# Kernel optimization log

Hardware: AMD Instinct MI355X
Metric: run time of the kernel (lower is better)

Reference implementation:

```python
import jax, jax.numpy as jnp
import numpy as np

# dims: M=512 new tokens, N=2048 model dim, D=128 head dim, H=16 heads,
# L=4096 cache length, P=2048 cache write offset

def setup_inputs() -> dict:
    key = jax.random.key(0)
    k0, k1, k2, k3 = jax.random.split(key, 4)
    M, N, D, L = 512, 2048, 128, 4096
    X = jax.random.normal(k0, (M, N), jnp.float32)
    # scale weights ~1/sqrt(N) so projections have unit-ish scale
    W_qkv = jax.random.normal(k1, (N, 3 * N), jnp.float32) * (N ** -0.5)
    H = N // D
    cache_K = jax.random.normal(k2, (H, L, D), jnp.float32)
    # realistic cache state: keys stored in cache are RMS-normalized
    cache_K = cache_K * jax.lax.rsqrt(jnp.mean(cache_K * cache_K, axis=-1, keepdims=True))
    cache_V = jax.random.normal(k3, (H, L, D), jnp.float32)
    return {"X": X, "W_qkv": W_qkv, "cache_K": cache_K, "cache_V": cache_V, "P": 2048}


def reference(X, W_qkv, cache_K, cache_V, P):
    M = X.shape[0]
    H, L, D = cache_K.shape
    qkv = X @ W_qkv                              # [M, 3N]
    q, k, v = jnp.split(qkv, 3, axis=-1)         # each [M, N]
    q = q.reshape(M, H, D).transpose(1, 0, 2)    # [H, M, D]
    k = k.reshape(M, H, D).transpose(1, 0, 2)
    v = v.reshape(M, H, D).transpose(1, 0, 2)
    # RMS-style normalization (no learned gain, no eps in original)
    q = q * jax.lax.rsqrt(jnp.mean(q * q, axis=-1, keepdims=True))
    k = k * jax.lax.rsqrt(jnp.mean(k * k, axis=-1, keepdims=True))
    # scatter-update into KV cache at position P
    Kc = jax.lax.dynamic_update_slice(cache_K, k, (0, P, 0))  # [H, L, D]
    Vc = jax.lax.dynamic_update_slice(cache_V, v, (0, P, 0))
    # unmasked, unscaled attention over the full cache (faithful to original:
    # plain exp/sum, no max-subtraction, no 1/sqrt(D))
    scores = jnp.einsum('hmd,hld->hml', q, Kc)   # [H, M, L]
    w = jnp.exp(scores)
    w = w / jnp.sum(w, axis=-1, keepdims=True)
    out = jnp.einsum('hml,hld->hmd', w, Vc)      # [H, M, D]
    return out.transpose(1, 0, 2).reshape(M, H * D)
```

## Files before the change

kernel.cpp:

```cpp
#include <hip/hip_runtime.h>
#include <math.h>

typedef _Float16 half_t;
typedef _Float16 half8 __attribute__((ext_vector_type(8)));
typedef _Float16 half4_t __attribute__((ext_vector_type(4)));
typedef _Float16 half2_t __attribute__((ext_vector_type(2)));
typedef float floatx4 __attribute__((ext_vector_type(4)));

#define M_TOK 512
#define N_DIM 2048
#define D_HEAD 128
#define H_HEADS 16
#define L_CACHE 4096
#define THREE_N 6144
#define NCHUNK 8
#define LCHUNK 512

__global__ __launch_bounds__(256) void prep_kernel(const float* __restrict__ W,
                                                   const float* __restrict__ X,
                                                   half_t* __restrict__ W16T,
                                                   half_t* __restrict__ X16) {
    __shared__ half_t tile[64 * 66];
    int b = blockIdx.x;
    int t = threadIdx.x;

    if (b < 3072) {
        int n0 = (b % 96) * 64, k0 = (b / 96) * 64;
        {
            int k = t >> 2, c0 = (t & 3) * 16;
            const float* src = W + (size_t)(k0 + k) * THREE_N + n0 + c0;
            float4 v[4];
#pragma unroll
            for (int j = 0; j < 4; ++j) v[j] = *(const float4*)(src + j * 4);
#pragma unroll
            for (int j = 0; j < 4; ++j) {
                tile[(c0 + j * 4 + 0) * 66 + k] = (half_t)v[j].x;
                tile[(c0 + j * 4 + 1) * 66 + k] = (half_t)v[j].y;
                tile[(c0 + j * 4 + 2) * 66 + k] = (half_t)v[j].z;
                tile[(c0 + j * 4 + 3) * 66 + k] = (half_t)v[j].w;
            }
        }
        __syncthreads();
        {
            int n = t >> 2, kg = (t & 3) * 16;
            half_t* dst = W16T + (size_t)(n0 + n) * N_DIM + k0 + kg;
            *(half8*)(dst) = *(half8*)&tile[n * 66 + kg];
            *(half8*)(dst + 8) = *(half8*)&tile[n * 66 + kg + 8];
        }
        return;
    }
    b -= 3072;
    {
        size_t i = (size_t)b * 2048 + t * 4;
        float4 v0 = *(const float4*)(X + i);
        float4 v1 = *(const float4*)(X + i + 1024);
        half4_t h0 = {(half_t)v0.x, (half_t)v0.y, (half_t)v0.z, (half_t)v0.w};
        half4_t h1 = {(half_t)v1.x, (half_t)v1.y, (half_t)v1.z, (half_t)v1.w};
        *(half4_t*)(X16 + i) = h0;
        *(half4_t*)(X16 + i + 1024) = h1;
    }
}

__global__ __launch_bounds__(256, 5) void mega_kernel(const half_t* __restrict__ X16,
                                                      const half_t* __restrict__ W16T,
                                                      const float* __restrict__ cK,
                                                      const float* __restrict__ cV,
                                                      const int* __restrict__ Pp,
                                                      half_t* __restrict__ Q16,
                                                      half_t* __restrict__ K16,
                                                      half_t* __restrict__ V16T) {
    __shared__ __align__(16) char smem[20992];
    const int t = threadIdx.x;
    int b = blockIdx.x;

    if (b >= 768) {
        b -= 768;
        const int P = *Pp;
        if (b < 1024) {
            int h = b >> 6, l0 = (b & 63) * 64;
            if (l0 >= P && l0 + 64 <= P + M_TOK) return;
            size_t base = ((size_t)h * L_CACHE + l0) * D_HEAD;
            float4 v[8];
#pragma unroll
            for (int i = 0; i < 8; ++i)
                v[i] = *(const float4*)(cK + base + i * 1024 + t * 4);
#pragma unroll
            for (int i = 0; i < 8; ++i) {
                int row = l0 + ((i * 1024 + t * 4) >> 7);
                half4_t hh = {(half_t)v[i].x, (half_t)v[i].y, (half_t)v[i].z, (half_t)v[i].w};
                if (row < P || row >= P + M_TOK)
                    *(half4_t*)(K16 + base + i * 1024 + t * 4) = hh;
            }
            return;
        }
        b -= 1024;
        {
            int h = b >> 7;
            int rem = b & 127;
            int lt = rem >> 1, dt = rem & 1;
            int l0 = lt * 64, d0 = dt * 64;
            if (l0 >= P && l0 + 64 <= P + M_TOK) return;
            bool overlap = (l0 < P + M_TOK) && (l0 + 64 > P);
            half_t* tile = (half_t*)smem;
            {
                int l = t >> 2, c0 = (t & 3) * 16;
                const float* src = cV + ((size_t)h * L_CACHE + l0 + l) * D_HEAD + d0 + c0;
                float4 v[4];
#pragma unroll
                for (int j = 0; j < 4; ++j) v[j] = *(const float4*)(src + j * 4);
#pragma unroll
                for (int j = 0; j < 4; ++j) {
                    tile[(c0 + j * 4 + 0) * 66 + l] = (half_t)v[j].x;
                    tile[(c0 + j * 4 + 1) * 66 + l] = (half_t)v[j].y;
                    tile[(c0 + j * 4 + 2) * 66 + l] = (half_t)v[j].z;
                    tile[(c0 + j * 4 + 3) * 66 + l] = (half_t)v[j].w;
                }
            }
            __syncthreads();
            {
                int d = t >> 2, lg = (t & 3) * 16;
                half_t* dst = V16T + ((size_t)h * D_HEAD + d0 + d) * L_CACHE + l0 + lg;
                if (!overlap) {
                    *(half8*)(dst) = *(half8*)&tile[d * 66 + lg];
                    *(half8*)(dst + 8) = *(half8*)&tile[d * 66 + lg + 8];
                } else {
#pragma unroll
                    for (int j = 0; j < 16; ++j) {
                        int l = l0 + lg + j;
                        if (l < P || l >= P + M_TOK) dst[j] = tile[d * 66 + lg + j];
                    }
                }
            }
            return;
        }
    }

    half_t* As = (half_t*)smem;
    half_t* Bs = (half_t*)(smem + 4096);
    half_t* Vt = (half_t*)smem;
    float* ssb = (float*)(smem + 20480);
    const int wid = t >> 6, lane = t & 63;
    const int quad = lane >> 4, ln = lane & 15;
    const int bx = b % 48, by = b / 48;
    const int m0 = by * 32, n0 = bx * 128;
    const int wm = (wid >> 1) * 16, wn = (wid & 1) * 64;

    floatx4 acc[4] = {};

    const int ar = t >> 3, ag = (t & 7) * 8;
    const int br = t >> 3, bg = (t & 7) * 8;
    const int rdk = (ln & 7) << 3;

    for (int k0 = 0; k0 < N_DIM; k0 += 64) {
        __syncthreads();
        *(half8*)&As[ar * 64 + (ag ^ ((ar & 7) << 3))] =
            *(const half8*)(X16 + (size_t)(m0 + ar) * N_DIM + k0 + ag);
#pragma unroll
        for (int p = 0; p < 4; ++p) {
            int r = br + p * 32;
            *(half8*)&Bs[r * 64 + (bg ^ ((r & 7) << 3))] =
                *(const half8*)(W16T + (size_t)(n0 + r) * N_DIM + k0 + bg);
        }
        __syncthreads();
#pragma unroll
        for (int kt = 0; kt < 2; ++kt) {
            half8 a, bb[4];
            a = *(half8*)&As[(wm + ln) * 64 + ((kt * 32 + quad * 8) ^ rdk)];
#pragma unroll
            for (int j = 0; j < 4; ++j)
                bb[j] = *(half8*)&Bs[(wn + j * 16 + ln) * 64 + ((kt * 32 + quad * 8) ^ rdk)];
#pragma unroll
            for (int j = 0; j < 4; ++j)
                acc[j] = __builtin_amdgcn_mfma_f32_16x16x32_f16(a, bb[j], acc[j], 0, 0, 0);
        }
    }

    const int seg = bx >> 4, h = bx & 15;
    const int P = *Pp;

    if (seg < 2) {
        float ss[4], scale[4];
#pragma unroll
        for (int r = 0; r < 4; ++r) {
            float s = 0.f;
#pragma unroll
            for (int j = 0; j < 4; ++j) s += acc[j][r] * acc[j][r];
#pragma unroll
            for (int msk = 1; msk < 16; msk <<= 1) s += __shfl_xor(s, msk, 64);
            ss[r] = s;
        }
        if (ln == 0) {
#pragma unroll
            for (int r = 0; r < 4; ++r)
                ssb[wid * 16 + quad * 4 + r] = ss[r];
        }
        __syncthreads();
#pragma unroll
        for (int r = 0; r < 4; ++r)
            scale[r] = rsqrtf((ss[r] + ssb[(wid ^ 1) * 16 + quad * 4 + r]) * (1.0f / 128.0f));
#pragma unroll
        for (int j = 0; j < 4; ++j) {
            int col = wn + j * 16 + ln;
#pragma unroll
            for (int r = 0; r < 4; ++r) {
                int m = m0 + wm + quad * 4 + r;
                half_t val = (half_t)(acc[j][r] * scale[r]);
                if (seg == 0)
                    Q16[((size_t)h * M_TOK + m) * D_HEAD + col] = val;
                else
                    K16[((size_t)h * L_CACHE + P + m) * D_HEAD + col] = val;
            }
        }
    } else {
        __syncthreads();
#pragma unroll
        for (int j = 0; j < 4; ++j) {
            int d = wn + j * 16 + ln;
#pragma unroll
            for (int r = 0; r < 4; ++r)
                Vt[d * 40 + wm + quad * 4 + r] = (half_t)acc[j][r];
        }
        __syncthreads();
#pragma unroll
        for (int p = 0; p < 2; ++p) {
            int s = p * 256 + t;
            int d = s >> 2, sg = s & 3;
            *(half8*)(V16T + ((size_t)h * D_HEAD + d) * L_CACHE + P + m0 + sg * 8) =
                *(half8*)&Vt[d * 40 + sg * 8];
        }
    }
}

__global__ __launch_bounds__(256, 4) void attn_partial_kernel(const half_t* __restrict__ Q16,
                                                              const half_t* __restrict__ K16,
                                                              const half_t* __restrict__ V16T,
                                                              half_t* __restrict__ Opart,
                                                              float* __restrict__ mstat,
                                                              float* __restrict__ lstat) {
    __shared__ half_t Ks[64 * 128];
    __shared__ half_t Vs[128 * 64];
    __shared__ half_t Ps[4 * 16 * 64];
    const int t = threadIdx.x, w = t >> 6, lane = t & 63;
    const int quad = lane >> 4, ln = lane & 15;

    const int bid = blockIdx.x;
    const int xcd = bid & 7, slot = bid >> 3;
    const int pair = (xcd << 4) | (slot >> 3);
    const int h = pair & 15, c = pair >> 4, mi = slot & 7;
    const int mb = mi * 64;

    const half_t* Qh = Q16 + (size_t)h * M_TOK * D_HEAD;
    const half_t* Kh = K16 + (size_t)h * L_CACHE * D_HEAD;
    const half_t* Vh = V16T + (size_t)h * D_HEAD * L_CACHE;

    const int m0 = mb + w * 16;
    half8 qf[4];
#pragma unroll
    for (int dt = 0; dt < 4; ++dt)
        qf[dt] = *(const half8*)(Qh + (size_t)(m0 + ln) * D_HEAD + dt * 32 + quad * 8);

    floatx4 oacc[8] = {};
    float mrow = -INFINITY;
    float lrow = 0.f;

    half_t* Pw = Ps + w * (16 * 64);
    const int psw = (ln & 7) << 3;

    const int l0base = c * LCHUNK;
    const int kr = t >> 4, kc = (t & 15) * 8;
    const int vr = t >> 3, vc = (t & 7) * 8;
    const int ksw = (kr & 7) << 3;
    const int vsw = (vr & 7) << 3;

    half8 kreg[4], vreg[4];
#pragma unroll
    for (int p = 0; p < 4; ++p) {
        kreg[p] = *(const half8*)(Kh + (size_t)(l0base + p * 16 + kr) * D_HEAD + kc);
        vreg[p] = *(const half8*)(Vh + (size_t)(p * 32 + vr) * L_CACHE + l0base + vc);
    }

    for (int it = 0; it < LCHUNK / 64; ++it) {
        __syncthreads();
#pragma unroll
        for (int p = 0; p < 4; ++p)
            *(half8*)&Ks[(p * 16 + kr) * 128 + (kc ^ ksw)] = kreg[p];
#pragma unroll
        for (int p = 0; p < 4; ++p)
            *(half8*)&Vs[(p * 32 + vr) * 64 + (vc ^ vsw)] = vreg[p];
        if (it + 1 < LCHUNK / 64) {
            int l1 = l0base + (it + 1) * 64;
#pragma unroll
            for (int p = 0; p < 4; ++p) {
                kreg[p] = *(const half8*)(Kh + (size_t)(l1 + p * 16 + kr) * D_HEAD + kc);
                vreg[p] = *(const half8*)(Vh + (size_t)(p * 32 + vr) * L_CACHE + l1 + vc);
            }
        }
        __syncthreads();

        floatx4 sacc[4] = {};
#pragma unroll
        for (int dt = 0; dt < 4; ++dt) {
            half8 kf[4];
#pragma unroll
            for (int nt = 0; nt < 4; ++nt)
                kf[nt] = *(half8*)&Ks[(nt * 16 + ln) * 128 + ((dt * 32 + quad * 8) ^ psw)];
#pragma unroll
            for (int nt = 0; nt < 4; ++nt)
                sacc[nt] = __builtin_amdgcn_mfma_f32_16x16x32_f16(kf[nt], qf[dt], sacc[nt], 0, 0, 0);
        }

        {
            float mx = sacc[0][0];
#pragma unroll
            for (int nt = 0; nt < 4; ++nt)
#pragma unroll
                for (int r = 0; r < 4; ++r) mx = fmaxf(mx, sacc[nt][r]);
            mx = fmaxf(mx, __shfl_xor(mx, 16));
            mx = fmaxf(mx, __shfl_xor(mx, 32));
            if (__ballot(mx > mrow)) {
                float mnew = fmaxf(mrow, mx);
                float alpha = __expf(mrow - mnew);
                mrow = mnew;
                lrow *= alpha;
                float ar[4];
#pragma unroll
                for (int r = 0; r < 4; ++r) ar[r] = __shfl(alpha, quad * 4 + r, 16);
#pragma unroll
                for (int nt8 = 0; nt8 < 8; ++nt8)
#pragma unroll
                    for (int r = 0; r < 4; ++r) oacc[nt8][r] *= ar[r];
            }
            float psum = 0.f;
#pragma unroll
            for (int nt = 0; nt < 4; ++nt) {
                half4_t h4;
#pragma unroll
                for (int r = 0; r < 4; ++r) {
                    float p = __expf(sacc[nt][r] - mrow);
                    psum += p;
                    h4[r] = (half_t)p;
                }
                *(half4_t*)&Pw[ln * 64 + ((nt * 16 + quad * 4) ^ psw)] = h4;
            }
            psum += __shfl_xor(psum, 16);
            psum += __shfl_xor(psum, 32);
            lrow += psum;
        }

#pragma unroll
        for (int kt = 0; kt < 2; ++kt) {
            half8 a = *(half8*)&Pw[ln * 64 + ((kt * 32 + quad * 8) ^ psw)];
#pragma unroll
            for (int nt8 = 0; nt8 < 8; ++nt8) {
                half8 b = *(half8*)&Vs[(nt8 * 16 + ln) * 64 + ((kt * 32 + quad * 8) ^ psw)];
                oacc[nt8] = __builtin_amdgcn_mfma_f32_16x16x32_f16(a, b, oacc[nt8], 0, 0, 0);
            }
        }
    }

    half_t* Oc = Opart + ((size_t)(c * H_HEADS + h) * M_TOK) * D_HEAD;
    float* ms = mstat + (size_t)(c * H_HEADS + h) * M_TOK;
    float* ls = lstat + (size_t)(c * H_HEADS + h) * M_TOK;
#pragma unroll
    for (int nt8 = 0; nt8 < 8; ++nt8) {
        int col = nt8 * 16 + ln;
#pragma unroll
        for (int r = 0; r < 4; ++r)
            Oc[(size_t)(m0 + quad * 4 + r) * D_HEAD + col] = (half_t)oacc[nt8][r];
    }
    if (lane < 16) {
        ms[m0 + lane] = mrow;
        ls[m0 + lane] = lrow;
    }
}

__global__ __launch_bounds__(256) void combine_kernel(const half_t* __restrict__ Opart,
                                                      const float* __restrict__ mstat,
                                                      const float* __restrict__ lstat,
                                                      float* __restrict__ out) {
    int gw = blockIdx.x * 4 + (threadIdx.x >> 6);
    int lane = threadIdx.x & 63;
    int h = gw >> 9, m = gw & 511;
    int d = lane * 2;

    float ms[NCHUNK];
    float mg = -INFINITY;
#pragma unroll
    for (int c = 0; c < NCHUNK; ++c) {
        ms[c] = mstat[((c * H_HEADS + h) << 9) + m];
        mg = fmaxf(mg, ms[c]);
    }
    float denom = 0.f, o0 = 0.f, o1 = 0.f;
#pragma unroll
    for (int c = 0; c < NCHUNK; ++c) {
        float e = __expf(ms[c] - mg);
        denom += lstat[((c * H_HEADS + h) << 9) + m] * e;
        const half_t* Oc = Opart + (((size_t)(c * H_HEADS + h) << 9) + m) * D_HEAD + d;
        half2_t v = *(const half2_t*)Oc;
        o0 += (float)v.x * e;
        o1 += (float)v.y * e;
    }
    float inv = 1.0f / denom;
    float* op = out + (size_t)m * N_DIM + h * D_HEAD + d;
    op[0] = o0 * inv;
    op[1] = o1 * inv;
}

extern "C" void kernel_launch(void* const* d_in, const int* in_sizes, int n_in,
                              void* d_out, int out_size, void* d_ws, size_t ws_size,
                              hipStream_t stream) {
    const float* X = (const float*)d_in[0];
    const float* W = (const float*)d_in[1];
    const float* cK = (const float*)d_in[2];
    const float* cV = (const float*)d_in[3];
    const int* Pp = (const int*)d_in[4];
    float* out = (float*)d_out;

    char* ws = (char*)d_ws;
    half_t* Q16 = (half_t*)(ws + 0);
    half_t* K16 = (half_t*)(ws + 2097152);
    half_t* V16T = (half_t*)(ws + 18874368);
    half_t* X16 = (half_t*)(ws + 35651584);
    half_t* W16T = (half_t*)(ws + 37748736);
    half_t* Opart = (half_t*)(ws + 37748736);
    float* mstat = (float*)(ws + 71303168);
    float* lstat = (float*)(ws + 71827456);

    prep_kernel<<<3584, 256, 0, stream>>>(W, X, W16T, X16);
    mega_kernel<<<3840, 256, 0, stream>>>(X16, W16T, cK, cV, Pp, Q16, K16, V16T);
    attn_partial_kernel<<<1024, 256, 0, stream>>>(Q16, K16, V16T, Opart, mstat, lstat);
    combine_kernel<<<2048, 256, 0, stream>>>(Opart, mstat, lstat, out);
}
```

Before: 215.2 us.

## Fuse all stages into one persistent kernel with software grid barriers

Replaces the four separate launches (prep, GEMM+cache convert, attention partial, combine) with a single persistent kernel of 512 blocks that loops over work units and separates stages with atomic-based grid barriers. Within the middle stage, blocks interleave GEMM and cache-conversion work in alternating order so memory-bound and compute-bound work overlap across the device. The aim is to remove launch gaps and tail effects between kernels. In exchange, occupancy is capped at 512 resident blocks with larger shared memory, the barriers spin-wait, and the scheme relies on all blocks being co-resident to avoid deadlock.

```diff
diff --git a/kernel.cpp b/kernel.cpp
--- a/kernel.cpp
+++ b/kernel.cpp
@@ -15,395 +15,436 @@
 #define THREE_N 6144
 #define NCHUNK 8
 #define LCHUNK 512
-
-__global__ __launch_bounds__(256) void prep_kernel(const float* __restrict__ W,
-                                                   const float* __restrict__ X,
-                                                   half_t* __restrict__ W16T,
-                                                   half_t* __restrict__ X16) {
-    __shared__ half_t tile[64 * 66];
-    int b = blockIdx.x;
-    int t = threadIdx.x;
-
-    if (b < 3072) {
-        int n0 = (b % 96) * 64, k0 = (b / 96) * 64;
-        {
-            int k = t >> 2, c0 = (t & 3) * 16;
-            const float* src = W + (size_t)(k0 + k) * THREE_N + n0 + c0;
-            float4 v[4];
-#pragma unroll
-            for (int j = 0; j < 4; ++j) v[j] = *(const float4*)(src + j * 4);
-#pragma unroll
-            for (int j = 0; j < 4; ++j) {
-                tile[(c0 + j * 4 + 0) * 66 + k] = (half_t)v[j].x;
-                tile[(c0 + j * 4 + 1) * 66 + k] = (half_t)v[j].y;
-                tile[(c0 + j * 4 + 2) * 66 + k] = (half_t)v[j].z;
-                tile[(c0 + j * 4 + 3) * 66 + k] = (half_t)v[j].w;
-            }
+#define NBLK 512
+
+__device__ __forceinline__ void grid_bar(int* cnt, int* gen, int k) {
+    __syncthreads();
+    if (threadIdx.x == 0) {
+        int prev = __hip_atomic_fetch_add(cnt, 1, __ATOMIC_ACQ_REL, __HIP_MEMORY_SCOPE_AGENT);
+        if (prev == NBLK - 1) {
+            __hip_atomic_store(cnt, 0, __ATOMIC_RELAXED, __HIP_MEMORY_SCOPE_AGENT);
+            __hip_atomic_store(gen, k + 1, __ATOMIC_RELEASE, __HIP_MEMORY_SCOPE_AGENT);
+        } else {
+            while (__hip_atomic_load(gen, __ATOMIC_RELAXED, __HIP_MEMORY_SCOPE_AGENT) <= k)
+                __builtin_amdgcn_s_sleep(16);
+        }
+        __builtin_amdgcn_fence(__ATOMIC_ACQUIRE, "agent");
+    }
+    __syncthreads();
+}
+
+__global__ __launch_bounds__(256, 2) void fused_kernel(
+    const float* __restrict__ X, const float* __restrict__ W,
+    const float* __restrict__ cK, const float* __restrict__ cV,
+    const int* __restrict__ Pp,
+    half_t* __restrict__ W16T, half_t* __restrict__ X16,
+    half_t* __restrict__ Q16, half_t* __restrict__ K16,
+    half_t* __restrict__ V16T,
+    half_t* __restrict__ Opart, float* __restrict__ mstat,
+    float* __restrict__ lstat, float* __restrict__ out,
+    int* bar_cnt, int* bar_gen) {
+    __shared__ __align__(16) char smem[40960];
+    const int t = threadIdx.x;
+    const int bid = blockIdx.x;
+
+    {
+        half_t* tile = (half_t*)smem;
+        for (int u = bid; u < 3584; u += NBLK) {
+            if (u < 3072) {
+                int n0 = (u % 96) * 64, k0 = (u / 96) * 64;
+                __syncthreads();
+                {
+                    int k = t >> 2, c0 = (t & 3) * 16;
+                    const float* src = W + (size_t)(k0 + k) * THREE_N + n0 + c0;
+                    float4 v[4];
+#pragma unroll
+                    for (int j = 0; j < 4; ++j) v[j] = *(const float4*)(src + j * 4);
+#pragma unroll
+                    for (int j = 0; j < 4; ++j) {
+                        tile[(c0 + j * 4 + 0) * 66 + k] = (half_t)v[j].x;
+                        tile[(c0 + j * 4 + 1) * 66 + k] = (half_t)v[j].y;
+                        tile[(c0 + j * 4 + 2) * 66 + k] = (half_t)v[j].z;
+                        tile[(c0 + j * 4 + 3) * 66 + k] = (half_t)v[j].w;
+                    }
+                }
+                __syncthreads();
+                {
+                    int n = t >> 2, kg = (t & 3) * 16;
+                    half_t* dst = W16T + (size_t)(n0 + n) * N_DIM + k0 + kg;
+                    *(half8*)(dst) = *(half8*)&tile[n * 66 + kg];
+                    *(half8*)(dst + 8) = *(half8*)&tile[n * 66 + kg + 8];
+                }
+            } else {
+                int b = u - 3072;
+                size_t i = (size_t)b * 2048 + t * 4;
+                float4 v0 = *(const float4*)(X + i);
+                float4 v1 = *(const float4*)(X + i + 1024);
+                half4_t h0 = {(half_t)v0.x, (half_t)v0.y, (half_t)v0.z, (half_t)v0.w};
+                half4_t h1 = {(half_t)v1.x, (half_t)v1.y, (half_t)v1.z, (half_t)v1.w};
+                *(half4_t*)(X16 + i) = h0;
+                *(half4_t*)(X16 + i + 1024) = h1;
+            }
+        }
+    }
+    grid_bar(bar_cnt, bar_gen, 0);
+
+    {
+        const int P = *Pp;
+
+        auto conv_units = [&]() {
+#pragma unroll 1
+            for (int k = 0; k < 6; ++k) {
+                int u = bid * 6 + k;
+                if (u < 1024) {
+                    int h = u >> 6, l0 = (u & 63) * 64;
+                    if (l0 >= P && l0 + 64 <= P + M_TOK) continue;
+                    size_t base = ((size_t)h * L_CACHE + l0) * D_HEAD;
+                    float4 v[8];
+#pragma unroll
+                    for (int i = 0; i < 8; ++i)
+                        v[i] = *(const float4*)(cK + base + i * 1024 + t * 4);
+#pragma unroll
+                    for (int i = 0; i < 8; ++i) {
+                        int row = l0 + ((i * 1024 + t * 4) >> 7);
+                        half4_t hh = {(half_t)v[i].x, (half_t)v[i].y,
+                                      (half_t)v[i].z, (half_t)v[i].w};
+                        if (row < P || row >= P + M_TOK)
+                            *(half4_t*)(K16 + base + i * 1024 + t * 4) = hh;
+                    }
+                } else {
+                    int b = u - 1024;
+                    int h = b >> 7;
+                    int rem = b & 127;
+                    int lt = rem >> 1, dt = rem & 1;
+                    int l0 = lt * 64, d0 = dt * 64;
+                    if (l0 >= P && l0 + 64 <= P + M_TOK) continue;
+                    bool overlap = (l0 < P + M_TOK) && (l0 + 64 > P);
+                    half_t* tile = (half_t*)smem;
+                    __syncthreads();
+                    {
+                        int l = t >> 2, c0 = (t & 3) * 16;
+                        const float* src =
+                            cV + ((size_t)h * L_CACHE + l0 + l) * D_HEAD + d0 + c0;
+                        float4 v[4];
+#pragma unroll
+                        for (int j = 0; j < 4; ++j) v[j] = *(const float4*)(src + j * 4);
+#pragma unroll
+                        for (int j = 0; j < 4; ++j) {
+                            tile[(c0 + j * 4 + 0) * 66 + l] = (half_t)v[j].x;
+                            tile[(c0 + j * 4 + 1) * 66 + l] = (half_t)v[j].y;
+                            tile[(c0 + j * 4 + 2) * 66 + l] = (half_t)v[j].z;
+                            tile[(c0 + j * 4 + 3) * 66 + l] = (half_t)v[j].w;
+                        }
+                    }
+                    __syncthreads();
+                    {
+                        int d = t >> 2, lg = (t & 3) * 16;
+                        half_t* dst =
+                            V16T + ((size_t)h * D_HEAD + d0 + d) * L_CACHE + l0 + lg;
+                        if (!overlap) {
+                            *(half8*)(dst) = *(half8*)&tile[d * 66 + lg];
+                            *(half8*)(dst + 8) = *(half8*)&tile[d * 66 + lg + 8];
+                        } else {
+#pragma unroll
+                            for (int j = 0; j < 16; ++j) {
+                                int l = l0 + lg + j;
+                                if (l < P || l >= P + M_TOK)
+                                    dst[j] = tile[d * 66 + lg + j];
+                            }
+                        }
+                    }
+                }
+            }
+        };
+
+        auto gemm_units = [&]() {
+#pragma unroll 1
+            for (int u = bid; u < 768; u += NBLK) {
+                half_t* As = (half_t*)smem;
+                half_t* Bs = (half_t*)(smem + 4096);
+                half_t* Vt = (half_t*)smem;
+                float* ssb = (float*)(smem + 20480);
+                const int wid = t >> 6, lane = t & 63;
+                const int quad = lane >> 4, ln = lane & 15;
+                const int bx = u % 48, by = u / 48;
+                const int m0 = by * 32, n0 = bx * 128;
+                const int wm = (wid >> 1) * 16, wn = (wid & 1) * 64;
+
+                floatx4 acc[4] = {};
+
+                const int ar = t >> 3, ag = (t & 7) * 8;
+                const int br = t >> 3, bg = (t & 7) * 8;
+                const int rdk = (ln & 7) << 3;
+
+                for (int k0 = 0; k0 < N_DIM; k0 += 64) {
+                    __syncthreads();
+                    *(half8*)&As[ar * 64 + (ag ^ ((ar & 7) << 3))] =
+                        *(const half8*)(X16 + (size_t)(m0 + ar) * N_DIM + k0 + ag);
+#pragma unroll
+                    for (int p = 0; p < 4; ++p) {
+                        int r = br + p * 32;
+                        *(half8*)&Bs[r * 64 + (bg ^ ((r & 7) << 3))] =
+                            *(const half8*)(W16T + (size_t)(n0 + r) * N_DIM + k0 + bg);
+                    }
+                    __syncthreads();
+#pragma unroll
+                    for (int kt = 0; kt < 2; ++kt) {
+                        half8 a, bb[4];
+                        a = *(half8*)&As[(wm + ln) * 64 + ((kt * 32 + quad * 8) ^ rdk)];
+#pragma unroll
+                        for (int j = 0; j < 4; ++j)
+                            bb[j] = *(half8*)&Bs[(wn + j * 16 + ln) * 64 +
+                                                 ((kt * 32 + quad * 8) ^ rdk)];
+#pragma unroll
+                        for (int j = 0; j < 4; ++j)
+                            acc[j] = __builtin_amdgcn_mfma_f32_16x16x32_f16(
+                                a, bb[j], acc[j], 0, 0, 0);
+                    }
+                }
+
+                const int seg = bx >> 4, h = bx & 15;
+
+                if (seg < 2) {
+                    float ss[4], scale[4];
+#pragma unroll
+                    for (int r = 0; r < 4; ++r) {
+                        float s = 0.f;
+#pragma unroll
+                        for (int j = 0; j < 4; ++j) s += acc[j][r] * acc[j][r];
+#pragma unroll
+                        for (int msk = 1; msk < 16; msk <<= 1) s += __shfl_xor(s, msk, 64);
+                        ss[r] = s;
+                    }
+                    if (ln == 0) {
+#pragma unroll
+                        for (int r = 0; r < 4; ++r)
+                            ssb[wid * 16 + quad * 4 + r] = ss[r];
+                    }
+                    __syncthreads();
+#pragma unroll
+                    for (int r = 0; r < 4; ++r)
+                        scale[r] = rsqrtf((ss[r] + ssb[(wid ^ 1) * 16 + quad * 4 + r]) *
+                                          (1.0f / 128.0f));
+#pragma unroll
+                    for (int j = 0; j < 4; ++j) {
+                        int col = wn + j * 16 + ln;
+#pragma unroll
+                        for (int r = 0; r < 4; ++r) {
+                            int m = m0 + wm + quad * 4 + r;
+                            half_t val = (half_t)(acc[j][r] * scale[r]);
+                            if (seg == 0)
+                                Q16[((size_t)h * M_TOK + m) * D_HEAD + col] = val;
+                            else
+                                K16[((size_t)h * L_CACHE + P + m) * D_HEAD + col] = val;
+                        }
+                    }
+                    __syncthreads();
+                } else {
+                    __syncthreads();
+#pragma unroll
+                    for (int j = 0; j < 4; ++j) {
+                        int d = wn + j * 16 + ln;
+#pragma unroll
+                        for (int r = 0; r < 4; ++r)
+                            Vt[d * 40 + wm + quad * 4 + r] = (half_t)acc[j][r];
+                    }
+                    __syncthreads();
+#pragma unroll
+                    for (int p = 0; p < 2; ++p) {
+                        int s = p * 256 + t;
+                        int d = s >> 2, sg = s & 3;
+                        *(half8*)(V16T + ((size_t)h * D_HEAD + d) * L_CACHE + P + m0 +
+                                  sg * 8) = *(half8*)&Vt[d * 40 + sg * 8];
+                    }
+                    __syncthreads();
+                }
+            }
+        };
+
+        if ((bid + (bid >> 8)) & 1) {
+            gemm_units();
+            conv_units();
+        } else {
+            conv_units();
+            gemm_units();
+        }
+    }
+    grid_bar(bar_cnt, bar_gen, 1);
+
+#pragma unroll 1
+    for (int u3 = bid; u3 < 1024; u3 += NBLK) {
+        half_t* Ks = (half_t*)smem;
+        half_t* Vs = (half_t*)(smem + 16384);
+        half_t* Ps = (half_t*)(smem + 32768);
+        const int w = t >> 6, lane = t & 63;
+        const int quad = lane >> 4, ln = lane & 15;
+
+        const int xcd = u3 & 7, slot = u3 >> 3;
+        const int pair = (xcd << 4) | (slot >> 3);
+        const int h = pair & 15, c = pair >> 4, mi = slot & 7;
+        const int mb = mi * 64;
+
+        const half_t* Qh = Q16 + (size_t)h * M_TOK * D_HEAD;
+        const half_t* Kh = K16 + (size_t)h * L_CACHE * D_HEAD;
+        const half_t* Vh = V16T + (size_t)h * D_HEAD * L_CACHE;
+
+        const int m0 = mb + w * 16;
+        half8 qf[4];
+#pragma unroll
+        for (int dt = 0; dt < 4; ++dt)
+            qf[dt] = *(const half8*)(Qh + (size_t)(m0 + ln) * D_HEAD + dt * 32 + quad * 8);
+
+        floatx4 oacc[8] = {};
+        float mrow = -INFINITY;
+        float lrow = 0.f;
+
+        half_t* Pw = Ps + w * (16 * 64);
+        const int psw = (ln & 7) << 3;
+
+        const int l0base = c * LCHUNK;
+        const int kr = t >> 4, kc = (t & 15) * 8;
+        const int vr = t >> 3, vc = (t & 7) * 8;
+        const int ksw = (kr & 7) << 3;
+        const int vsw = (vr & 7) << 3;
+
+        half8 kreg[4], vreg[4];
+#pragma unroll
+        for (int p = 0; p < 4; ++p) {
+            kreg[p] = *(const half8*)(Kh + (size_t)(l0base + p * 16 + kr) * D_HEAD + kc);
+            vreg[p] = *(const half8*)(Vh + (size_t)(p * 32 + vr) * L_CACHE + l0base + vc);
+        }
+
+        for (int it = 0; it < LCHUNK / 64; ++it) {
+            __syncthreads();
+#pragma unroll
+            for (int p = 0; p < 4; ++p)
+                *(half8*)&Ks[(p * 16 + kr) * 128 + (kc ^ ksw)] = kreg[p];
+#pragma unroll
+            for (int p = 0; p < 4; ++p)
+                *(half8*)&Vs[(p * 32 + vr) * 64 + (vc ^ vsw)] = vreg[p];
+            if (it + 1 < LCHUNK / 64) {
+                int l1 = l0base + (it + 1) * 64;
+#pragma unroll
+                for (int p = 0; p < 4; ++p) {
+                    kreg[p] = *(const half8*)(Kh + (size_t)(l1 + p * 16 + kr) * D_HEAD + kc);
+                    vreg[p] = *(const half8*)(Vh + (size_t)(p * 32 + vr) * L_CACHE + l1 + vc);
+                }
+            }
+            __syncthreads();
+
+            floatx4 sacc[4] = {};
+#pragma unroll
+            for (int dt = 0; dt < 4; ++dt) {
+                half8 kf[4];
+#pragma unroll
+                for (int nt = 0; nt < 4; ++nt)
+                    kf[nt] = *(half8*)&Ks[(nt * 16 + ln) * 128 +
+                                          ((dt * 32 + quad * 8) ^ psw)];
+#pragma unroll
+                for (int nt = 0; nt < 4; ++nt)
+                    sacc[nt] = __builtin_amdgcn_mfma_f32_16x16x32_f16(kf[nt], qf[dt],
+                                                                      sacc[nt], 0, 0, 0);
+            }
+
+            {
+                float mx = sacc[0][0];
+#pragma unroll
+                for (int nt = 0; nt < 4; ++nt)
+#pragma unroll
+                    for (int r = 0; r < 4; ++r) mx = fmaxf(mx, sacc[nt][r]);
+                mx = fmaxf(mx, __shfl_xor(mx, 16));
+                mx = fmaxf(mx, __shfl_xor(mx, 32));
+                if (__ballot(mx > mrow)) {
+                    float mnew = fmaxf(mrow, mx);
+                    float alpha = __expf(mrow - mnew);
+                    mrow = mnew;
+                    lrow *= alpha;
+                    float ar4[4];
+#pragma unroll
+                    for (int r = 0; r < 4; ++r) ar4[r] = __shfl(alpha, quad * 4 + r, 16);
+#pragma unroll
+                    for (int nt8 = 0; nt8 < 8; ++nt8)
+#pragma unroll
+                        for (int r = 0; r < 4; ++r) oacc[nt8][r] *= ar4[r];
+                }
+                float psum = 0.f;
+#pragma unroll
+                for (int nt = 0; nt < 4; ++nt) {
+                    half4_t h4;
+#pragma unroll
+                    for (int r = 0; r < 4; ++r) {
+                        float p = __expf(sacc[nt][r] - mrow);
+                        psum += p;
+                        h4[r] = (half_t)p;
+                    }
+                    *(half4_t*)&Pw[ln * 64 + ((nt * 16 + quad * 4) ^ psw)] = h4;
+                }
+                psum += __shfl_xor(psum, 16);
+                psum += __shfl_xor(psum, 32);
+                lrow += psum;
+            }
+
+#pragma unroll
+            for (int kt = 0; kt < 2; ++kt) {
+                half8 a = *(half8*)&Pw[ln * 64 + ((kt * 32 + quad * 8) ^ psw)];
+#pragma unroll
+                for (int nt8 = 0; nt8 < 8; ++nt8) {
+                    half8 b = *(half8*)&Vs[(nt8 * 16 + ln) * 64 +
+                                           ((kt * 32 + quad * 8) ^ psw)];
+                    oacc[nt8] = __builtin_amdgcn_mfma_f32_16x16x32_f16(a, b, oacc[nt8],
+                                                                       0, 0, 0);
+                }
+            }
+        }
+
+        half_t* Oc = Opart + ((size_t)(c * H_HEADS + h) * M_TOK) * D_HEAD;
+        float* ms = mstat + (size_t)(c * H_HEADS + h) * M_TOK;
+        float* ls = lstat + (size_t)(c * H_HEADS + h) * M_TOK;
+#pragma unroll
+        for (int nt8 = 0; nt8 < 8; ++nt8) {
+            int col = nt8 * 16 + ln;
+#pragma unroll
+            for (int r = 0; r < 4; ++r)
+                Oc[(size_t)(m0 + quad * 4 + r) * D_HEAD + col] = (half_t)oacc[nt8][r];
+        }
+        if (lane < 16) {
+            ms[m0 + lane] = mrow;
+            ls[m0 + lane] = lrow;
         }
         __syncthreads();
-        {
-            int n = t >> 2, kg = (t & 3) * 16;
-            half_t* dst = W16T + (size_t)(n0 + n) * N_DIM + k0 + kg;
-            *(half8*)(dst) = *(half8*)&tile[n * 66 + kg];
-            *(half8*)(dst + 8) = *(half8*)&tile[n * 66 + kg + 8];
-        }
-        return;
     }
-    b -= 3072;
-    {
-        size_t i = (size_t)b * 2048 + t * 4;
-        float4 v0 = *(const float4*)(X + i);
-        float4 v1 = *(const float4*)(X + i + 1024);
-        half4_t h0 = {(half_t)v0.x, (half_t)v0.y, (half_t)v0.z, (half_t)v0.w};
-        half4_t h1 = {(half_t)v1.x, (half_t)v1.y, (half_t)v1.z, (half_t)v1.w};
-        *(half4_t*)(X16 + i) = h0;
-        *(half4_t*)(X16 + i + 1024) = h1;
+    grid_bar(bar_cnt, bar_gen, 2);
+
+#pragma unroll 1
+    for (int u = bid; u < 2048; u += NBLK) {
+        int gw = u * 4 + (t >> 6);
+        int lane = t & 63;
+        int h = gw >> 9, m = gw & 511;
+        int d = lane * 2;
+
+        float ms[NCHUNK];
+        float mg = -INFINITY;
+#pragma unroll
+        for (int c = 0; c < NCHUNK; ++c) {
+            ms[c] = mstat[((c * H_HEADS + h) << 9) + m];
+            mg = fmaxf(mg, ms[c]);
+        }
+        float denom = 0.f, o0 = 0.f, o1 = 0.f;
+#pragma unroll
+        for (int c = 0; c < NCHUNK; ++c) {
+            float e = __expf(ms[c] - mg);
+            denom += lstat[((c * H_HEADS + h) << 9) + m] * e;
+            const half_t* Oc =
+                Opart + (((size_t)(c * H_HEADS + h) << 9) + m) * D_HEAD + d;
+            half2_t v = *(const half2_t*)Oc;
+            o0 += (float)v.x * e;
+            o1 += (float)v.y * e;
+        }
+        float inv = 1.0f / denom;
+        float* op = out + (size_t)m * N_DIM + h * D_HEAD + d;
+        op[0] = o0 * inv;
+        op[1] = o1 * inv;
     }
-}
-
-__global__ __launch_bounds__(256, 5) void mega_kernel(const half_t* __restrict__ X16,
-                                                      const half_t* __restrict__ W16T,
-                                                      const float* __restrict__ cK,
-                                                      const float* __restrict__ cV,
-                                                      const int* __restrict__ Pp,
-                                                      half_t* __restrict__ Q16,
-                                                      half_t* __restrict__ K16,
-                                                      half_t* __restrict__ V16T) {
-    __shared__ __align__(16) char smem[20992];
-    const int t = threadIdx.x;
-    int b = blockIdx.x;
-
-    if (b >= 768) {
-        b -= 768;
-        const int P = *Pp;
-        if (b < 1024) {
-            int h = b >> 6, l0 = (b & 63) * 64;
-            if (l0 >= P && l0 + 64 <= P + M_TOK) return;
-            size_t base = ((size_t)h * L_CACHE + l0) * D_HEAD;
-            float4 v[8];
-#pragma unroll
-            for (int i = 0; i < 8; ++i)
-                v[i] = *(const float4*)(cK + base + i * 1024 + t * 4);
-#pragma unroll
-            for (int i = 0; i < 8; ++i) {
-                int row = l0 + ((i * 1024 + t * 4) >> 7);
-                half4_t hh = {(half_t)v[i].x, (half_t)v[i].y, (half_t)v[i].z, (half_t)v[i].w};
-                if (row < P || row >= P + M_TOK)
-                    *(half4_t*)(K16 + base + i * 1024 + t * 4) = hh;
-            }
-            return;
-        }
-        b -= 1024;
-        {
-            int h = b >> 7;
-            int rem = b & 127;
-            int lt = rem >> 1, dt = rem & 1;
-            int l0 = lt * 64, d0 = dt * 64;
-            if (l0 >= P && l0 + 64 <= P + M_TOK) return;
-            bool overlap = (l0 < P + M_TOK) && (l0 + 64 > P);
-            half_t* tile = (half_t*)smem;
-            {
-                int l = t >> 2, c0 = (t & 3) * 16;
-                const float* src = cV + ((size_t)h * L_CACHE + l0 + l) * D_HEAD + d0 + c0;
-                float4 v[4];
-#pragma unroll
-                for (int j = 0; j < 4; ++j) v[j] = *(const float4*)(src + j * 4);
-#pragma unroll
-                for (int j = 0; j < 4; ++j) {
-                    tile[(c0 + j * 4 + 0) * 66 + l] = (half_t)v[j].x;
-                    tile[(c0 + j * 4 + 1) * 66 + l] = (half_t)v[j].y;
-                    tile[(c0 + j * 4 + 2) * 66 + l] = (half_t)v[j].z;
-                    tile[(c0 + j * 4 + 3) * 66 + l] = (half_t)v[j].w;
-                }
-            }
-            __syncthreads();
-            {
-                int d = t >> 2, lg = (t & 3) * 16;
-                half_t* dst = V16T + ((size_t)h * D_HEAD + d0 + d) * L_CACHE + l0 + lg;
-                if (!overlap) {
-                    *(half8*)(dst) = *(half8*)&tile[d * 66 + lg];
-                    *(half8*)(dst + 8) = *(half8*)&tile[d * 66 + lg + 8];
-                } else {
-#pragma unroll
-                    for (int j = 0; j < 16; ++j) {
-                        int l = l0 + lg + j;
-                        if (l < P || l >= P + M_TOK) dst[j] = tile[d * 66 + lg + j];
-                    }
-                }
-            }
-            return;
-        }
-    }
-
-    half_t* As = (half_t*)smem;
-    half_t* Bs = (half_t*)(smem + 4096);
-    half_t* Vt = (half_t*)smem;
-    float* ssb = (float*)(smem + 20480);
-    const int wid = t >> 6, lane = t & 63;
-    const int quad = lane >> 4, ln = lane & 15;
-    const int bx = b % 48, by = b / 48;
-    const int m0 = by * 32, n0 = bx * 128;
-    const int wm = (wid >> 1) * 16, wn = (wid & 1) * 64;
-
-    floatx4 acc[4] = {};
-
-    const int ar = t >> 3, ag = (t & 7) * 8;
-    const int br = t >> 3, bg = (t & 7) * 8;
-    const int rdk = (ln & 7) << 3;
-
-    for (int k0 = 0; k0 < N_DIM; k0 += 64) {
-        __syncthreads();
-        *(half8*)&As[ar * 64 + (ag ^ ((ar & 7) << 3))] =
-            *(const half8*)(X16 + (size_t)(m0 + ar) * N_DIM + k0 + ag);
-#pragma unroll
-        for (int p = 0; p < 4; ++p) {
-            int r = br + p * 32;
-            *(half8*)&Bs[r * 64 + (bg ^ ((r & 7) << 3))] =
-                *(const half8*)(W16T + (size_t)(n0 + r) * N_DIM + k0 + bg);
-        }
-        __syncthreads();
-#pragma unroll
-        for (int kt = 0; kt < 2; ++kt) {
-            half8 a, bb[4];
-            a = *(half8*)&As[(wm + ln) * 64 + ((kt * 32 + quad * 8) ^ rdk)];
-#pragma unroll
-            for (int j = 0; j < 4; ++j)
-                bb[j] = *(half8*)&Bs[(wn + j * 16 + ln) * 64 + ((kt * 32 + quad * 8) ^ rdk)];
-#pragma unroll
-            for (int j = 0; j < 4; ++j)
-                acc[j] = __builtin_amdgcn_mfma_f32_16x16x32_f16(a, bb[j], acc[j], 0, 0, 0);
-        }
-    }
-
-    const int seg = bx >> 4, h = bx & 15;
-    const int P = *Pp;
-
-    if (seg < 2) {
-        float ss[4], scale[4];
-#pragma unroll
-        for (int r = 0; r < 4; ++r) {
-            float s = 0.f;
-#pragma unroll
-            for (int j = 0; j < 4; ++j) s += acc[j][r] * acc[j][r];
-#pragma unroll
-            for (int msk = 1; msk < 16; msk <<= 1) s += __shfl_xor(s, msk, 64);
-            ss[r] = s;
-        }
-        if (ln == 0) {
-#pragma unroll
-            for (int r = 0; r < 4; ++r)
-                ssb[wid * 16 + quad * 4 + r] = ss[r];
-        }
-        __syncthreads();
-#pragma unroll
-        for (int r = 0; r < 4; ++r)
-            scale[r] = rsqrtf((ss[r] + ssb[(wid ^ 1) * 16 + quad * 4 + r]) * (1.0f / 128.0f));
-#pragma unroll
-        for (int j = 0; j < 4; ++j) {
-            int col = wn + j * 16 + ln;
-#pragma unroll
-            for (int r = 0; r < 4; ++r) {
-                int m = m0 + wm + quad * 4 + r;
-                half_t val = (half_t)(acc[j][r] * scale[r]);
-                if (seg == 0)
-                    Q16[((size_t)h * M_TOK + m) * D_HEAD + col] = val;
-                else
-                    K16[((size_t)h * L_CACHE + P + m) * D_HEAD + col] = val;
-            }
-        }
-    } else {
-        __syncthreads();
-#pragma unroll
-        for (int j = 0; j < 4; ++j) {
-            int d = wn + j * 16 + ln;
-#pragma unroll
-            for (int r = 0; r < 4; ++r)
-                Vt[d * 40 + wm + quad * 4 + r] = (half_t)acc[j][r];
-        }
-        __syncthreads();
-#pragma unroll
-        for (int p = 0; p < 2; ++p) {
-            int s = p * 256 + t;
-            int d = s >> 2, sg = s & 3;
-            *(half8*)(V16T + ((size_t)h * D_HEAD + d) * L_CACHE + P + m0 + sg * 8) =
-                *(half8*)&Vt[d * 40 + sg * 8];
-        }
-    }
-}
-
-__global__ __launch_bounds__(256, 4) void attn_partial_kernel(const half_t* __restrict__ Q16,
-                                                              const half_t* __restrict__ K16,
-                                                              const half_t* __restrict__ V16T,
-                                                              half_t* __restrict__ Opart,
-                                                              float* __restrict__ mstat,
-                                                              float* __restrict__ lstat) {
-    __shared__ half_t Ks[64 * 128];
-    __shared__ half_t Vs[128 * 64];
-    __shared__ half_t Ps[4 * 16 * 64];
-    const int t = threadIdx.x, w = t >> 6, lane = t & 63;
-    const int quad = lane >> 4, ln = lane & 15;
-
-    const int bid = blockIdx.x;
-    const int xcd = bid & 7, slot = bid >> 3;
-    const int pair = (xcd << 4) | (slot >> 3);
-    const int h = pair & 15, c = pair >> 4, mi = slot & 7;
-    const int mb = mi * 64;
-
-    const half_t* Qh = Q16 + (size_t)h * M_TOK * D_HEAD;
-    const half_t* Kh = K16 + (size_t)h * L_CACHE * D_HEAD;
-    const half_t* Vh = V16T + (size_t)h * D_HEAD * L_CACHE;
-
-    const int m0 = mb + w * 16;
-    half8 qf[4];
-#pragma unroll
-    for (int dt = 0; dt < 4; ++dt)
-        qf[dt] = *(const half8*)(Qh + (size_t)(m0 + ln) * D_HEAD + dt * 32 + quad * 8);
-
-    floatx4 oacc[8] = {};
-    float mrow = -INFINITY;
-    float lrow = 0.f;
-
-    half_t* Pw = Ps + w * (16 * 64);
-    const int psw = (ln & 7) << 3;
-
-    const int l0base = c * LCHUNK;
-    const int kr = t >> 4, kc = (t & 15) * 8;
-    const int vr = t >> 3, vc = (t & 7) * 8;
-    const int ksw = (kr & 7) << 3;
-    const int vsw = (vr & 7) << 3;
-
-    half8 kreg[4], vreg[4];
-#pragma unroll
-    for (int p = 0; p < 4; ++p) {
-        kreg[p] = *(const half8*)(Kh + (size_t)(l0base + p * 16 + kr) * D_HEAD + kc);
-        vreg[p] = *(const half8*)(Vh + (size_t)(p * 32 + vr) * L_CACHE + l0base + vc);
-    }
-
-    for (int it = 0; it < LCHUNK / 64; ++it) {
-        __syncthreads();
-#pragma unroll
-        for (int p = 0; p < 4; ++p)
-            *(half8*)&Ks[(p * 16 + kr) * 128 + (kc ^ ksw)] = kreg[p];
-#pragma unroll
-        for (int p = 0; p < 4; ++p)
-            *(half8*)&Vs[(p * 32 + vr) * 64 + (vc ^ vsw)] = vreg[p];
-        if (it + 1 < LCHUNK / 64) {
-            int l1 = l0base + (it + 1) * 64;
-#pragma unroll
-            for (int p = 0; p < 4; ++p) {
-                kreg[p] = *(const half8*)(Kh + (size_t)(l1 + p * 16 + kr) * D_HEAD + kc);
-                vreg[p] = *(const half8*)(Vh + (size_t)(p * 32 + vr) * L_CACHE + l1 + vc);
-            }
-        }
-        __syncthreads();
-
-        floatx4 sacc[4] = {};
-#pragma unroll
-        for (int dt = 0; dt < 4; ++dt) {
-            half8 kf[4];
-#pragma unroll
-            for (int nt = 0; nt < 4; ++nt)
-                kf[nt] = *(half8*)&Ks[(nt * 16 + ln) * 128 + ((dt * 32 + quad * 8) ^ psw)];
-#pragma unroll
-            for (int nt = 0; nt < 4; ++nt)
-                sacc[nt] = __builtin_amdgcn_mfma_f32_16x16x32_f16(kf[nt], qf[dt], sacc[nt], 0, 0, 0);
-        }
-
-        {
-            float mx = sacc[0][0];
-#pragma unroll
-            for (int nt = 0; nt < 4; ++nt)
-#pragma unroll
-                for (int r = 0; r < 4; ++r) mx = fmaxf(mx, sacc[nt][r]);
-            mx = fmaxf(mx, __shfl_xor(mx, 16));
-            mx = fmaxf(mx, __shfl_xor(mx, 32));
-            if (__ballot(mx > mrow)) {
-                float mnew = fmaxf(mrow, mx);
-                float alpha = __expf(mrow - mnew);
-                mrow = mnew;
-                lrow *= alpha;
-                float ar[4];
-#pragma unroll
-                for (int r = 0; r < 4; ++r) ar[r] = __shfl(alpha, quad * 4 + r, 16);
-#pragma unroll
-                for (int nt8 = 0; nt8 < 8; ++nt8)
-#pragma unroll
-                    for (int r = 0; r < 4; ++r) oacc[nt8][r] *= ar[r];
-            }
-            float psum = 0.f;
-#pragma unroll
-            for (int nt = 0; nt < 4; ++nt) {
-                half4_t h4;
-#pragma unroll
-                for (int r = 0; r < 4; ++r) {
-                    float p = __expf(sacc[nt][r] - mrow);
-                    psum += p;
-                    h4[r] = (half_t)p;
-                }
-                *(half4_t*)&Pw[ln * 64 + ((nt * 16 + quad * 4) ^ psw)] = h4;
-            }
-            psum += __shfl_xor(psum, 16);
-            psum += __shfl_xor(psum, 32);
-            lrow += psum;
-        }
-
-#pragma unroll
-        for (int kt = 0; kt < 2; ++kt) {
-            half8 a = *(half8*)&Pw[ln * 64 + ((kt * 32 + quad * 8) ^ psw)];
-#pragma unroll
-            for (int nt8 = 0; nt8 < 8; ++nt8) {
-                half8 b = *(half8*)&Vs[(nt8 * 16 + ln) * 64 + ((kt * 32 + quad * 8) ^ psw)];
-                oacc[nt8] = __builtin_amdgcn_mfma_f32_16x16x32_f16(a, b, oacc[nt8], 0, 0, 0);
-            }
-        }
-    }
-
-    half_t* Oc = Opart + ((size_t)(c * H_HEADS + h) * M_TOK) * D_HEAD;
-    float* ms = mstat + (size_t)(c * H_HEADS + h) * M_TOK;
-    float* ls = lstat + (size_t)(c * H_HEADS + h) * M_TOK;
-#pragma unroll
-    for (int nt8 = 0; nt8 < 8; ++nt8) {
-        int col = nt8 * 16 + ln;
-#pragma unroll
-        for (int r = 0; r < 4; ++r)
-            Oc[(size_t)(m0 + quad * 4 + r) * D_HEAD + col] = (half_t)oacc[nt8][r];
-    }
-    if (lane < 16) {
-        ms[m0 + lane] = mrow;
-        ls[m0 + lane] = lrow;
-    }
-}
-
-__global__ __launch_bounds__(256) void combine_kernel(const half_t* __restrict__ Opart,
-                                                      const float* __restrict__ mstat,
-                                                      const float* __restrict__ lstat,
-                                                      float* __restrict__ out) {
-    int gw = blockIdx.x * 4 + (threadIdx.x >> 6);
-    int lane = threadIdx.x & 63;
-    int h = gw >> 9, m = gw & 511;
-    int d = lane * 2;
-
-    float ms[NCHUNK];
-    float mg = -INFINITY;
-#pragma unroll
-    for (int c = 0; c < NCHUNK; ++c) {
-        ms[c] = mstat[((c * H_HEADS + h) << 9) + m];
-        mg = fmaxf(mg, ms[c]);
-    }
-    float denom = 0.f, o0 = 0.f, o1 = 0.f;
-#pragma unroll
-    for (int c = 0; c < NCHUNK; ++c) {
-        float e = __expf(ms[c] - mg);
-        denom += lstat[((c * H_HEADS + h) << 9) + m] * e;
-        const half_t* Oc = Opart + (((size_t)(c * H_HEADS + h) << 9) + m) * D_HEAD + d;
-        half2_t v = *(const half2_t*)Oc;
-        o0 += (float)v.x * e;
-        o1 += (float)v.y * e;
-    }
-    float inv = 1.0f / denom;
-    float* op = out + (size_t)m * N_DIM + h * D_HEAD + d;
-    op[0] = o0 * inv;
-    op[1] = o1 * inv;
 }
 
 extern "C" void kernel_launch(void* const* d_in, const int* in_sizes, int n_in,
@@ -425,9 +466,10 @@
     half_t* Opart = (half_t*)(ws + 37748736);
     float* mstat = (float*)(ws + 71303168);
     float* lstat = (float*)(ws + 71827456);
-
-    prep_kernel<<<3584, 256, 0, stream>>>(W, X, W16T, X16);
-    mega_kernel<<<3840, 256, 0, stream>>>(X16, W16T, cK, cV, Pp, Q16, K16, V16T);
-    attn_partial_kernel<<<1024, 256, 0, stream>>>(Q16, K16, V16T, Opart, mstat, lstat);
-    combine_kernel<<<2048, 256, 0, stream>>>(Opart, mstat, lstat, out);
+    int* bar = (int*)(ws + 72351680);
+
+    hipMemsetAsync(bar, 0, 16, stream);
+    fused_kernel<<<NBLK, 256, 0, stream>>>(X, W, cK, cV, Pp, W16T, X16, Q16, K16,
+                                           V16T, Opart, mstat, lstat, out, bar,
+                                           bar + 1);
 }
```

Measured after the change: 373.6 us. 1.74x slower.
